# Kernel tuning notes

Measured on AMD Instinct MI355X. Metric: run time of the kernel, lower is better.

## Reference

```python
import jax, jax.numpy as jnp
import numpy as np

B, T, C = 8, 2048, 1024
HEAD_SIZE = 64
HEAD_NUM = 0
NUM_HEADS = 16


def setup_inputs() -> dict:
    key = jax.random.key(0)
    k1, k2, k3, k4 = jax.random.split(key, 4)
    x = jax.random.normal(k1, (B, T, C), dtype=jnp.float32)
    s = C ** -0.5  # Linear init scale
    Wq = jax.random.normal(k2, (C, HEAD_SIZE), dtype=jnp.float32) * s
    Wk = jax.random.normal(k3, (C, HEAD_SIZE), dtype=jnp.float32) * s
    Wv = jax.random.normal(k4, (C, HEAD_SIZE), dtype=jnp.float32) * s
    return {"x": x, "Wq": Wq, "Wk": Wk, "Wv": Wv}


def reference(x, Wq, Wk, Wv):
    # single head of self-attention with ALiBi bias + causal mask (dropout in eval mode = identity)
    q = x @ Wq  # [B,T,H]
    k = x @ Wk  # [B,T,H]
    v = x @ Wv  # [B,T,H]
    scale = jnp.float32(HEAD_SIZE) ** -0.5
    t = jnp.arange(T)
    # base_bias[i,j] = j - i, scaled by per-head ALiBi slope
    slope = 2.0 ** (-8.0 * (HEAD_NUM + 1) / NUM_HEADS)
    m = (t[None, :] - t[:, None]).astype(jnp.float32) * slope  # [T,T]
    # note: bias is added BEFORE the 1/sqrt(d) scaling, as in the original
    scores = (jnp.einsum('bqh,bkh->bqk', q, k) + m) * scale  # [B,T,T]
    causal = t[None, :] <= t[:, None]  # [T,T] lower-triangular
    scores = jnp.where(causal, scores, -jnp.inf)
    attn = jax.nn.softmax(scores, axis=-1)
    out = jnp.einsum('bqk,bkh->bqh', attn, v)  # [B,T,H]
    return out
```

## Files before the change

### kernel.cpp

```cpp
#include <hip/hip_runtime.h>
#include <hip/hip_bf16.h>
#include <math.h>

#define B_ 8
#define T_ 2048
#define C_ 1024
#define H_ 64
#define M_ (B_*T_)

typedef __attribute__((ext_vector_type(8))) short bf16x8;
typedef __attribute__((ext_vector_type(4))) float floatx4;

static __device__ __forceinline__ unsigned short f2bf(float f) {
    union { float f; unsigned u; } v; v.f = f;
    unsigned r = v.u + 0x7fffu + ((v.u >> 16) & 1u);
    return (unsigned short)(r >> 16);
}
static __device__ __forceinline__ unsigned short f2bf_fast(float f) {
    union { float f; unsigned u; } v; v.f = f;
    return (unsigned short)((v.u + 0x8000u) >> 16);
}
static __device__ __forceinline__ unsigned pk2h(float lo, float hi) {
    union { float f; unsigned u; } a, b; a.f = lo; b.f = hi;
    return __builtin_amdgcn_perm(b.u + 0x8000u, a.u + 0x8000u, 0x07060302u);
}
static __device__ __forceinline__ bf16x8 cvt8(float4 f0, float4 f1) {
    union { uint4 u; bf16x8 v; } r;
    r.u.x = pk2h(f0.x, f0.y); r.u.y = pk2h(f0.z, f0.w);
    r.u.z = pk2h(f1.x, f1.y); r.u.w = pk2h(f1.z, f1.w);
    return r.v;
}

#define MFMA(a,b,c) __builtin_amdgcn_mfma_f32_16x16x32_bf16((a),(b),(c),0,0,0)

__global__ __launch_bounds__(256) void wprep_kernel(
    const float* __restrict__ Wq, const float* __restrict__ Wk,
    const float* __restrict__ Wv, unsigned short* __restrict__ wt2)
{
    const int f    = blockIdx.x * 256 + threadIdx.x;
    const int nt   = f >> 11;
    const int kc   = (f >> 6) & 31;
    const int lane = f & 63;
    const int l15  = lane & 15, quad = lane >> 4;
    const int col  = nt * 16 + l15;
    const float* W = (col < 64) ? Wq : ((col < 128) ? Wk : Wv);
    const int   cw = col & 63;
    const float sc = (col < 64) ? 0.125f : 1.0f;
    unsigned short o[8];
    #pragma unroll
    for (int j = 0; j < 8; j++) {
        const int kk = kc * 32 + quad * 8 + j;
        o[j] = f2bf(W[(size_t)kk * 64 + cw] * sc);
    }
    *(uint4*)&wt2[(size_t)f * 8] = *(const uint4*)o;
}

__global__ __launch_bounds__(256) void qkv_kernel(
    const float* __restrict__ x, const unsigned short* __restrict__ wt2,
    unsigned short* __restrict__ qo, unsigned short* __restrict__ ko,
    unsigned short* __restrict__ vo)
{
    __shared__ __align__(16) unsigned short es[32 * 200];

    const int t    = threadIdx.x;
    const int w    = t >> 6;
    const int lane = t & 63;
    const int l15  = lane & 15;
    const int quad = lane >> 4;
    const int r0   = blockIdx.x * 32;

    floatx4 acc[2][3];
    #pragma unroll
    for (int m = 0; m < 2; m++)
        #pragma unroll
        for (int n = 0; n < 3; n++) acc[m][n] = (floatx4)(0.0f);

    const float*          xa = x   + (size_t)(r0 + l15) * C_ + quad * 8;
    const unsigned short* wb = wt2 + (size_t)(w * 3) * 32 * 512 + lane * 8;

    #pragma unroll 2
    for (int kc = 0; kc < 32; kc++) {
        const int k0 = kc * 32;
        const bf16x8 a0 = cvt8(*(const float4*)(xa + k0),
                               *(const float4*)(xa + k0 + 4));
        const bf16x8 a1 = cvt8(*(const float4*)(xa + 16 * C_ + k0),
                               *(const float4*)(xa + 16 * C_ + k0 + 4));
        const bf16x8 b0 = *(const bf16x8*)(wb + (size_t)(0 * 32 + kc) * 512);
        const bf16x8 b1 = *(const bf16x8*)(wb + (size_t)(1 * 32 + kc) * 512);
        const bf16x8 b2 = *(const bf16x8*)(wb + (size_t)(2 * 32 + kc) * 512);
        acc[0][0] = MFMA(a0, b0, acc[0][0]);
        acc[1][0] = MFMA(a1, b0, acc[1][0]);
        acc[0][1] = MFMA(a0, b1, acc[0][1]);
        acc[1][1] = MFMA(a1, b1, acc[1][1]);
        acc[0][2] = MFMA(a0, b2, acc[0][2]);
        acc[1][2] = MFMA(a1, b2, acc[1][2]);
    }

    #pragma unroll
    for (int mt = 0; mt < 2; mt++)
        #pragma unroll
        for (int nt = 0; nt < 3; nt++) {
            const int col = w * 48 + nt * 16 + l15;
            #pragma unroll
            for (int r = 0; r < 4; r++)
                es[(mt * 16 + quad * 4 + r) * 200 + col] = f2bf(acc[mt][nt][r]);
        }
    __syncthreads();

    {
        const int row = t >> 3, oct = t & 7;
        *(uint4*)&qo[(size_t)(r0 + row) * 64 + oct * 8] =
            *(const uint4*)&es[row * 200 + oct * 8];
        *(uint4*)&ko[(size_t)(r0 + row) * 64 + oct * 8] =
            *(const uint4*)&es[row * 200 + 64 + oct * 8];
    }
    {
        const int h = t >> 2, ts = (t & 3) * 8;
        const int bb = r0 >> 11, tt = r0 & 2047;
        unsigned short tmp[8];
        #pragma unroll
        for (int j = 0; j < 8; j++) tmp[j] = es[(ts + j) * 200 + 128 + h];
        *(uint4*)&vo[((size_t)bb * 64 + h) * 2048 + tt + ts] = *(uint4*)tmp;
    }
}

__global__ __launch_bounds__(256, 2) void attn_kernel(
    const unsigned short* __restrict__ q,
    const unsigned short* __restrict__ k,
    const unsigned short* __restrict__ vT,
    float* __restrict__ out)
{
    __shared__ __align__(16) unsigned char smem[16384 + 512];
    unsigned short* pT  = (unsigned short*)smem;
    float*          Omg = (float*)smem;
    float*          mlg = (float*)(smem + 16384);

    const int t    = threadIdx.x;
    const int w    = t >> 6;
    const int lane = t & 63;
    const int l15  = lane & 15;
    const int quad = lane >> 4;
    const int b    = blockIdx.x & 7;
    const int qt   = 127 - (blockIdx.x >> 3);
    const int q0   = qt * 16;
    const size_t kb = (size_t)b * T_ * 64;

    const bf16x8 qf0 = *(const bf16x8*)&q[kb + (size_t)(q0 + l15) * 64 + quad * 8];
    const bf16x8 qf1 = *(const bf16x8*)&q[kb + (size_t)(q0 + l15) * 64 + 32 + quad * 8];

    floatx4 O[4];
    #pragma unroll
    for (int i = 0; i < 4; i++) O[i] = (floatx4)(0.0f);
    float mrow[4], lrow[4];
    #pragma unroll
    for (int r = 0; r < 4; r++) { mrow[r] = -INFINITY; lrow[r] = 0.0f; }

    const int nk     = q0 + 16;
    const int nsteps = (nk + 63) >> 6;
    const int ns4    = (nsteps + 3) >> 2;
    const int sBeg   = w * ns4;
    const int sEnd   = min(sBeg + ns4, nsteps);
    const float bs   = 0.088388347648318447f;
    const int   ig0  = q0 + quad * 4;
    unsigned short* pw = pT + w * 16 * 72;

    for (int s = sBeg; s < sEnd; s++) {
        const int j0 = s * 64;

        bf16x8 kf[4][2], vf[4][2];
        #pragma unroll
        for (int nt = 0; nt < 4; nt++) {
            #pragma unroll
            for (int ks = 0; ks < 2; ks++) {
                kf[nt][ks] = *(const bf16x8*)
                    &k[kb + (size_t)(j0 + nt * 16 + l15) * 64 + ks * 32 + quad * 8];
                vf[nt][ks] = *(const bf16x8*)
                    &vT[((size_t)b * 64 + nt * 16 + l15) * 2048 + j0 + ks * 32 + quad * 8];
            }
        }

        floatx4 sc[4];
        #pragma unroll
        for (int nt = 0; nt < 4; nt++) {
            floatx4 z = (floatx4)(0.0f);
            z = MFMA(qf0, kf[nt][0], z);
            z = MFMA(qf1, kf[nt][1], z);
            sc[nt] = z;
        }

        #pragma unroll
        for (int r = 0; r < 4; r++) {
            const int ig = ig0 + r;
            float xv[4];
            float mloc = -INFINITY;
            #pragma unroll
            for (int nt = 0; nt < 4; nt++) {
                const int j = j0 + nt * 16 + l15;
                float v2 = sc[nt][r] + (float)(j - ig) * bs;
                if (j > ig) v2 = -INFINITY;
                xv[nt] = v2;
                mloc = fmaxf(mloc, v2);
            }
            #pragma unroll
            for (int off = 1; off < 16; off <<= 1)
                mloc = fmaxf(mloc, __shfl_xor(mloc, off));
            const float mnew = fmaxf(mrow[r], mloc);
            const float mq   = (mnew == -INFINITY) ? 0.0f : mnew;
            const float alpha = __expf(mrow[r] - mq);
            mrow[r] = mnew;
            float ps = 0.0f;
            #pragma unroll
            for (int nt = 0; nt < 4; nt++) {
                const float p = __expf(xv[nt] - mq);
                ps += p;
                pw[(quad * 4 + r) * 72 + nt * 16 + l15] = f2bf_fast(p);
            }
            lrow[r] = lrow[r] * alpha + ps;
            #pragma unroll
            for (int nt = 0; nt < 4; nt++) O[nt][r] *= alpha;
        }

        const bf16x8 pf0 = *(const bf16x8*)&pw[l15 * 72 + quad * 8];
        const bf16x8 pf1 = *(const bf16x8*)&pw[l15 * 72 + 32 + quad * 8];
        #pragma unroll
        for (int nt = 0; nt < 4; nt++) {
            O[nt] = MFMA(pf0, vf[nt][0], O[nt]);
            O[nt] = MFMA(pf1, vf[nt][1], O[nt]);
        }
    }

    #pragma unroll
    for (int r = 0; r < 4; r++)
        #pragma unroll
        for (int off = 1; off < 16; off <<= 1)
            lrow[r] += __shfl_xor(lrow[r], off);

    __syncthreads();

    #pragma unroll
    for (int nt = 0; nt < 4; nt++)
        #pragma unroll
        for (int r = 0; r < 4; r++)
            Omg[w * 1024 + (quad * 4 + r) * 64 + nt * 16 + l15] = O[nt][r];
    if (l15 == 0) {
        #pragma unroll
        for (int r = 0; r < 4; r++) {
            mlg[w * 32 + (quad * 4 + r)]      = mrow[r];
            mlg[w * 32 + 16 + (quad * 4 + r)] = lrow[r];
        }
    }
    __syncthreads();

    {
        const int row = t >> 4;
        const int hq  = (t & 15) << 2;
        float mstar = -INFINITY;
        #pragma unroll
        for (int w2 = 0; w2 < 4; w2++)
            mstar = fmaxf(mstar, mlg[w2 * 32 + row]);
        floatx4 oa = (floatx4)(0.0f);
        float lsum = 0.0f;
        #pragma unroll
        for (int w2 = 0; w2 < 4; w2++) {
            const float wg = __expf(mlg[w2 * 32 + row] - mstar);
            lsum += wg * mlg[w2 * 32 + 16 + row];
            const floatx4 ov = *(const floatx4*)&Omg[w2 * 1024 + row * 64 + hq];
            oa += wg * ov;
        }
        const float inv = 1.0f / lsum;
        *(floatx4*)&out[kb + (size_t)(q0 + row) * 64 + hq] = oa * inv;
    }
}

extern "C" void kernel_launch(void* const* d_in, const int* in_sizes, int n_in,
                              void* d_out, int out_size, void* d_ws, size_t ws_size,
                              hipStream_t stream) {
    (void)in_sizes; (void)n_in; (void)out_size; (void)ws_size;
    const float* x  = (const float*)d_in[0];
    const float* Wq = (const float*)d_in[1];
    const float* Wk = (const float*)d_in[2];
    const float* Wv = (const float*)d_in[3];
    float* out = (float*)d_out;

    unsigned short* wt2 = (unsigned short*)d_ws;
    unsigned short* qw  = wt2 + 196608;
    unsigned short* kw  = qw + (size_t)M_ * H_;
    unsigned short* vw  = kw + (size_t)M_ * H_;

    wprep_kernel<<<96, 256, 0, stream>>>(Wq, Wk, Wv, wt2);
    qkv_kernel<<<M_ / 32, 256, 0, stream>>>(x, wt2, qw, kw, vw);
    attn_kernel<<<B_ * 128, 256, 0, stream>>>(qw, kw, vw, out);
}
```

Measured before the change: 167.1 us.

## Prefetch next K/V tile in attention loop and fully unroll QKV projection

The attention kernel now loads the next step's K and V fragments into a second register set while the current step's softmax and PV MFMAs run, then copies them over at the end of the iteration. This hides global-memory latency behind compute. The QKV projection kernel's k-loop is fully unrolled, all loads are issued before the bf16 conversions, and it gets a min-2-blocks-per-CU launch bound. The cost is higher register pressure in both kernels, which could lower occupancy or cause spills.

```diff
diff --git a/kernel.cpp b/kernel.cpp
--- a/kernel.cpp
+++ b/kernel.cpp
@@ -55,7 +55,7 @@
     *(uint4*)&wt2[(size_t)f * 8] = *(const uint4*)o;
 }
 
-__global__ __launch_bounds__(256) void qkv_kernel(
+__global__ __launch_bounds__(256, 2) void qkv_kernel(
     const float* __restrict__ x, const unsigned short* __restrict__ wt2,
     unsigned short* __restrict__ qo, unsigned short* __restrict__ ko,
     unsigned short* __restrict__ vo)
@@ -75,19 +75,24 @@
         #pragma unroll
         for (int n = 0; n < 3; n++) acc[m][n] = (floatx4)(0.0f);
 
-    const float*          xa = x   + (size_t)(r0 + l15) * C_ + quad * 8;
-    const unsigned short* wb = wt2 + (size_t)(w * 3) * 32 * 512 + lane * 8;
-
-    #pragma unroll 2
+    const float*          xa0 = x   + (size_t)(r0 + l15) * C_ + quad * 8;
+    const float*          xa1 = xa0 + 16 * C_;
+    const unsigned short* wb0 = wt2 + (size_t)(w * 3 + 0) * 32 * 512 + lane * 8;
+    const unsigned short* wb1 = wt2 + (size_t)(w * 3 + 1) * 32 * 512 + lane * 8;
+    const unsigned short* wb2 = wt2 + (size_t)(w * 3 + 2) * 32 * 512 + lane * 8;
+
+    #pragma unroll
     for (int kc = 0; kc < 32; kc++) {
         const int k0 = kc * 32;
-        const bf16x8 a0 = cvt8(*(const float4*)(xa + k0),
-                               *(const float4*)(xa + k0 + 4));
-        const bf16x8 a1 = cvt8(*(const float4*)(xa + 16 * C_ + k0),
-                               *(const float4*)(xa + 16 * C_ + k0 + 4));
-        const bf16x8 b0 = *(const bf16x8*)(wb + (size_t)(0 * 32 + kc) * 512);
-        const bf16x8 b1 = *(const bf16x8*)(wb + (size_t)(1 * 32 + kc) * 512);
-        const bf16x8 b2 = *(const bf16x8*)(wb + (size_t)(2 * 32 + kc) * 512);
+        const float4 x00 = *(const float4*)(xa0 + k0);
+        const float4 x01 = *(const float4*)(xa0 + k0 + 4);
+        const float4 x10 = *(const float4*)(xa1 + k0);
+        const float4 x11 = *(const float4*)(xa1 + k0 + 4);
+        const bf16x8 b0  = *(const bf16x8*)(wb0 + (size_t)kc * 512);
+        const bf16x8 b1  = *(const bf16x8*)(wb1 + (size_t)kc * 512);
+        const bf16x8 b2  = *(const bf16x8*)(wb2 + (size_t)kc * 512);
+        const bf16x8 a0  = cvt8(x00, x01);
+        const bf16x8 a1  = cvt8(x10, x11);
         acc[0][0] = MFMA(a0, b0, acc[0][0]);
         acc[1][0] = MFMA(a1, b0, acc[1][0]);
         acc[0][1] = MFMA(a0, b1, acc[0][1]);
@@ -164,20 +169,23 @@
     const int   ig0  = q0 + quad * 4;
     unsigned short* pw = pT + w * 16 * 72;
 
+    bf16x8 kf[4][2], vf[4][2];
+    #define LOADSTEP(dK, dV, jj0)                                              \
+        { _Pragma("unroll")                                                    \
+          for (int nt = 0; nt < 4; nt++) {                                     \
+              _Pragma("unroll")                                                \
+              for (int ks = 0; ks < 2; ks++) {                                 \
+                  dK[nt][ks] = *(const bf16x8*)                                \
+                      &k[kb + (size_t)((jj0) + nt*16 + l15)*64 + ks*32 + quad*8]; \
+                  dV[nt][ks] = *(const bf16x8*)                                \
+                      &vT[((size_t)b*64 + nt*16 + l15)*2048 + (jj0) + ks*32 + quad*8]; \
+              } } }
+
+    if (sBeg < sEnd) LOADSTEP(kf, vf, sBeg * 64)
+
+    #pragma unroll 2
     for (int s = sBeg; s < sEnd; s++) {
         const int j0 = s * 64;
-
-        bf16x8 kf[4][2], vf[4][2];
-        #pragma unroll
-        for (int nt = 0; nt < 4; nt++) {
-            #pragma unroll
-            for (int ks = 0; ks < 2; ks++) {
-                kf[nt][ks] = *(const bf16x8*)
-                    &k[kb + (size_t)(j0 + nt * 16 + l15) * 64 + ks * 32 + quad * 8];
-                vf[nt][ks] = *(const bf16x8*)
-                    &vT[((size_t)b * 64 + nt * 16 + l15) * 2048 + j0 + ks * 32 + quad * 8];
-            }
-        }
 
         floatx4 sc[4];
         #pragma unroll
@@ -187,6 +195,10 @@
             z = MFMA(qf1, kf[nt][1], z);
             sc[nt] = z;
         }
+
+        bf16x8 kf2[4][2], vf2[4][2];
+        const bool more = (s + 1 < sEnd);
+        if (more) LOADSTEP(kf2, vf2, (s + 1) * 64)
 
         #pragma unroll
         for (int r = 0; r < 4; r++) {
@@ -227,7 +239,18 @@
             O[nt] = MFMA(pf0, vf[nt][0], O[nt]);
             O[nt] = MFMA(pf1, vf[nt][1], O[nt]);
         }
-    }
+
+        if (more) {
+            #pragma unroll
+            for (int nt = 0; nt < 4; nt++)
+                #pragma unroll
+                for (int ks = 0; ks < 2; ks++) {
+                    kf[nt][ks] = kf2[nt][ks];
+                    vf[nt][ks] = vf2[nt][ks];
+                }
+        }
+    }
+    #undef LOADSTEP
 
     #pragma unroll
     for (int r = 0; r < 4; r++)
```

New measurement: 172.9 us. +3.5%, slower.
